# Optimization experiments

Measured on AMD Instinct MI355X. Metric: run time of the kernel, lower is better.

The kernel has to match this reference:

```python
import jax, jax.numpy as jnp
import numpy as np

N = 8192          # num atoms
APM = 32          # atoms per molecule
M = N // APM      # 256 molecules
FEAT = 100        # hidden_channels == num_filters
NG = 25           # num gaussians
K = 28            # knn neighbors
L = 4             # num interaction blocks
CUTOFF = 6.0
LOG2 = float(np.log(2.0))


def ssp(x):
    # pyg ShiftedSoftplus: softplus(x) - log(2)
    return jax.nn.softplus(x) - LOG2


def setup_inputs() -> dict:
    key = jax.random.key(0)
    ks = jax.random.split(key, 16)
    z = jax.random.randint(ks[0], (N,), 1, 100)
    pos = jax.random.normal(ks[1], (N, 3), jnp.float32) * 2.0
    ptr = jnp.arange(0, N + APM, APM)  # [M+1] molecule boundaries

    def w(k, shape, fan):
        return (jax.random.normal(k, shape, jnp.float32) / np.sqrt(fan)).astype(jnp.float32)

    def b(k, shape):
        return jax.random.normal(k, shape, jnp.float32) * 0.01

    kb = jax.random.split(ks[15], 8)
    H = FEAT // 2
    return {
        "z": z,
        "pos": pos,
        "ptr": ptr,
        "emb": jax.random.normal(ks[2], (100, FEAT), jnp.float32),
        "mlp_w1": w(ks[3], (L, NG, FEAT), NG),
        "mlp_b1": b(kb[0], (L, FEAT)),
        "mlp_w2": w(ks[4], (L, FEAT, FEAT), FEAT),
        "mlp_b2": b(kb[1], (L, FEAT)),
        "lin1_w": w(ks[5], (L, FEAT, FEAT), FEAT),
        "lin2_w": w(ks[6], (L, FEAT, FEAT), FEAT),
        "lin2_b": b(kb[2], (L, FEAT)),
        "lin_w": w(ks[7], (L, FEAT, FEAT), FEAT),
        "lin_b": b(kb[3], (L, FEAT)),
        "out_w1": w(ks[8], (FEAT, H), FEAT),
        "out_b1": b(kb[4], (H,)),
        "out_w2": w(ks[9], (H, 1), H),
        "out_b2": b(kb[5], (1,)),
    }


def reference(z, pos, ptr, emb, mlp_w1, mlp_b1, mlp_w2, mlp_b2,
              lin1_w, lin2_w, lin2_b, lin_w, lin_b,
              out_w1, out_b1, out_w2, out_b2):
    n = z.shape[0]
    m = ptr.shape[0] - 1

    # ptr -> per-atom batch ids (index_fill + cumsum; OOB index N dropped)
    flag = jnp.zeros((n,), jnp.int32).at[ptr].set(1, mode="drop")
    flag = flag.at[0].set(0)
    batch = jnp.cumsum(flag)

    # ---- KNN interaction graph (full NxN pairwise distances + masking + topk)
    diff = pos[:, None, :] - pos[None, :, :]           # [N,N,3]
    d2 = jnp.sum(diff * diff, axis=-1)                  # [N,N]
    ar = jnp.arange(n)
    mask = (ar[:, None] == ar[None, :]) \
         | (batch[:, None] != batch[None, :]) \
         | (d2 > CUTOFF * CUTOFF)
    dist = jnp.where(mask, CUTOFF, jnp.sqrt(jnp.where(mask, 1.0, d2)))
    neg, idx = jax.lax.top_k(-dist, K)                  # k nearest per row
    ew = -neg.reshape(-1)                               # edge distances [N*K]
    src = idx.reshape(-1)                               # source atoms j; target of edge (i,m) is i

    # ---- Gaussian smearing
    offset = jnp.linspace(0.0, CUTOFF, NG)
    coeff = -0.5 / (offset[1] - offset[0]) ** 2
    ea = jnp.exp(coeff * (ew[:, None] - offset[None, :]) ** 2)  # [E,NG]

    # cosine cutoff (zero weight for padded edges at dist==cutoff)
    ccut = 0.5 * (jnp.cos(ew * jnp.pi / CUTOFF) + 1.0)          # [E]

    h = emb[z]                                                   # [N,F]
    f = h.shape[1]
    for l in range(L):
        # filter network on edge attributes
        Wf = ssp(ea @ mlp_w1[l] + mlp_b1[l]) @ mlp_w2[l] + mlp_b2[l]
        Wf = Wf * ccut[:, None]                                  # [E,F]
        # CFConv: lin1 -> gather*filter -> sum over k neighbors -> lin2
        x1 = h @ lin1_w[l]                                       # [N,F]
        msg = x1[src] * Wf                                       # [E,F]
        agg = msg.reshape(n, K, f).sum(axis=1)                   # each node i has exactly K incoming edges
        v = ssp(agg @ lin2_w[l] + lin2_b[l]) @ lin_w[l] + lin_b[l]
        h = h + v

    # readout head
    h = ssp(h @ out_w1 + out_b1)
    per_atom = (h @ out_w2 + out_b2).reshape(-1)                 # [N]
    return jax.ops.segment_sum(per_atom, batch, num_segments=m) # per-molecule energy [M]
```

## Files before the change

### kernel.cpp

```cpp
#include <hip/hip_runtime.h>
#include <math.h>

#define APM   32
#define NMOL  256
#define FEAT  100
#define NPAD  112
#define LAYERS 4
#define NTHREADS 1024
#define NWAVES   16
#define G_TBL 4096
#define TROW  128
#define X1STR 132
#define KEDGE 28

typedef _Float16 f16x8 __attribute__((ext_vector_type(8)));
typedef _Float16 f16x2 __attribute__((ext_vector_type(2)));
typedef float    f32x4 __attribute__((ext_vector_type(4)));
typedef float    f32x2 __attribute__((ext_vector_type(2)));

#define L1F_OFF 0
#define L2F_OFF 14336
#define LVF_OFF 28672
#define LWTOT   43008
#define WTOTAL  (4*LWTOT)

#define PREP_BLOCKS 672
#define TBL_BLOCKS  256

__device__ __forceinline__ float sspf(float x){
  return __logf(1.0f + __expf(x)) - 0.69314718056f;
}

__global__ __launch_bounds__(256) void prep_all(
    const float* __restrict__ lin1_w, const float* __restrict__ lin2_w,
    const float* __restrict__ lin_w,
    const float* __restrict__ mlp_w1, const float* __restrict__ mlp_b1,
    const float* __restrict__ mlp_w2, const float* __restrict__ mlp_b2,
    _Float16* __restrict__ outw, _Float16* __restrict__ tbn)
{
  if (blockIdx.x < PREP_BLOCKS){
    int gid = blockIdx.x*256 + threadIdx.x;
    int l = gid / LWTOT;
    int r = gid - l*LWTOT;
    const float* W; int e;
    if (r < 14336)      { W = lin1_w + l*10000; e = r; }
    else if (r < 28672) { W = lin2_w + l*10000; e = r - 14336; }
    else                { W = lin_w  + l*10000; e = r - 28672; }
    int j = e & 7, L = (e >> 3) & 63, tile = e >> 9;
    int kc = tile / 7, nt = tile - kc*7;
    int k = kc*32 + ((L >> 4) << 3) + j;
    int f = nt*16 + (L & 15);
    float v = (k < 100 && f < FEAT) ? W[k*FEAT + f] : 0.0f;
    outw[gid] = (_Float16)v;
    return;
  }
  __shared__ float sW2[10000];
  __shared__ float sW1[2500];
  __shared__ float sB1[100], sB2[100];
  __shared__ float sT[4][100];
  int bid = blockIdx.x - PREP_BLOCKS;
  int l = bid >> 6;
  int s0 = (bid & 63) * 64;
  int tid = threadIdx.x, wv = tid >> 6, lane = tid & 63;
  for (int i = tid; i < 10000; i += 256) sW2[i] = mlp_w2[l*10000 + i];
  for (int i = tid; i < 2500;  i += 256) sW1[i] = mlp_w1[l*2500 + i];
  if (tid < 100) sB1[tid] = mlp_b1[l*100 + tid];
  if (tid >= 128 && tid < 228) sB2[tid-128] = mlp_b2[l*100 + tid-128];
  __syncthreads();
  #pragma unroll 1
  for (int si = 0; si < 16; si++){
    int s = s0 + wv*16 + si;
    float d = 6.0f * (float)s / (float)(G_TBL - 1);
    float ea[25];
    #pragma unroll
    for (int g = 0; g < 25; g++){
      float u = d - 0.25f*(float)g;
      ea[g] = __expf(-8.0f*u*u);
    }
    #pragma unroll
    for (int kk = 0; kk < 2; kk++){
      int k = lane + kk*64;
      if (k < 100){
        float acc = sB1[k];
        #pragma unroll
        for (int g = 0; g < 25; g++)
          acc += ea[g] * sW1[g*100 + k];
        sT[wv][k] = sspf(acc);
      }
    }
    float cc = 0.5f*(__cosf(d*0.52359877559f) + 1.0f);
    #pragma unroll
    for (int ff = 0; ff < 2; ff++){
      int f = lane + ff*64;
      float val = 0.0f;
      if (f < 100){
        float o0=0.0f, o1=0.0f, o2=0.0f, o3=0.0f;
        #pragma unroll
        for (int k = 0; k < 100; k += 4){
          o0 += sT[wv][k  ] * sW2[(k  )*100 + f];
          o1 += sT[wv][k+1] * sW2[(k+1)*100 + f];
          o2 += sT[wv][k+2] * sW2[(k+2)*100 + f];
          o3 += sT[wv][k+3] * sW2[(k+3)*100 + f];
        }
        val = (sB2[f] + ((o0+o1)+(o2+o3))) * cc;
      }
      tbn[((size_t)l*G_TBL + s)*TROW + f] = (_Float16)val;
    }
  }
}

__global__ __launch_bounds__(1024)
__attribute__((amdgpu_waves_per_eu(4, 4)))
void schnet_mega(
    const int* __restrict__ z, const float* __restrict__ pos,
    const float* __restrict__ emb, const _Float16* __restrict__ wf,
    const _Float16* __restrict__ tbn,
    const float* __restrict__ lin2_b, const float* __restrict__ lin_b,
    const float* __restrict__ out_w1, const float* __restrict__ out_b1,
    const float* __restrict__ out_w2, const float* __restrict__ out_b2,
    float* __restrict__ out)
{
  __shared__ __align__(16) _Float16 sAf[APM*136];
  __shared__ __align__(16) _Float16 sBf[APM*136];
  __shared__ __align__(16) float    sX1[APM*X1STR];
  __shared__ __align__(16) float    sH [APM*NPAD];
  __shared__ float sD  [APM*33];
  __shared__ int   sOffC[APM*KEDGE];
  __shared__ int   sJx  [APM*KEDGE];
  __shared__ float sPos[96];
  __shared__ float sPart[NWAVES];

  int tid = threadIdx.x, lane = tid & 63, wv = tid >> 6;
  int q = lane >> 4, n = lane & 15;
  int mol = blockIdx.x, mb = mol*APM;

  if (tid < 96) sPos[tid] = pos[mb*3 + tid];
  if (tid < 512){
    int r0 = tid >> 4, c0 = 112 + (tid & 15);
    sBf[r0*136 + c0] = (_Float16)0.0f;
  }
  for (int i = tid; i < APM*20; i += NTHREADS){
    int r = i/20, c = 112 + (i - r*20);
    sX1[r*X1STR + c] = 0.0f;
  }
  for (int i = tid; i < APM*136; i += NTHREADS){
    int r = i/136, c = i - r*136;
    float v = (c < FEAT) ? emb[z[mb+r]*FEAT + c] : 0.0f;
    sAf[i] = (_Float16)v;
    if (c < NPAD) sH[r*NPAD + c] = v;
  }
  __syncthreads();
  for (int p = tid; p < APM*APM; p += NTHREADS){
    int i = p >> 5, j = p & 31;
    float dx = sPos[i*3+0]-sPos[j*3+0];
    float dy = sPos[i*3+1]-sPos[j*3+1];
    float dz = sPos[i*3+2]-sPos[j*3+2];
    float d2 = dx*dx + dy*dy + dz*dz;
    sD[i*33+j] = (d2 > 36.0f) ? 6.0f : sqrtf(d2);
  }
  __syncthreads();
  if (tid < APM){
    float dd[32];
    #pragma unroll
    for (int j = 0; j < 32; j++) dd[j] = sD[tid*33+j];
    dd[tid] = 1e30f;
    unsigned dropped = 0u;
    for (int rr = 0; rr < 4; rr++){
      float mx = -1.0f; int mj = 0;
      #pragma unroll
      for (int j = 0; j < 32; j++){
        bool ok = !((dropped>>j)&1u) && (dd[j] > mx);
        mx = ok ? dd[j] : mx;  mj = ok ? j : mj;
      }
      dropped |= 1u << mj;
    }
    int e = 0;
    for (int j = 0; j < 32; j++){
      if ((dropped>>j)&1u) continue;
      float un = dd[j] * (float)((G_TBL-1)/6.0);
      int s = (int)(un + 0.5f);
      s = (s > G_TBL-1) ? (G_TBL-1) : s;
      sOffC[tid*KEDGE + e] = s*TROW;
      sJx  [tid*KEDGE + e] = j;
      e++;
    }
  }
  __syncthreads();

  for (int l = 0; l < LAYERS; l++){
    const _Float16* w1b = wf + l*LWTOT + L1F_OFF;
    const _Float16* w2b = wf + l*LWTOT + L2F_OFF;
    const _Float16* wvb = wf + l*LWTOT + LVF_OFF;
    const _Float16* tb = tbn + (size_t)l*G_TBL*TROW;
    for (int tau = wv; tau < 14; tau += NWAVES){
      int mt = tau/7, nt = tau - mt*7;
      f32x4 acc = {0.0f,0.0f,0.0f,0.0f};
      #pragma unroll
      for (int kc = 0; kc < 4; kc++){
        f16x8 av = *(const f16x8*)&sAf[(mt*16+n)*136 + kc*32 + q*8];
        f16x8 bv = *(const f16x8*)&w1b[((kc*7+nt)*64 + lane)*8];
        acc = __builtin_amdgcn_mfma_f32_16x16x32_f16(av, bv, acc, 0, 0, 0);
      }
      #pragma unroll
      for (int r = 0; r < 4; r++)
        sX1[(mt*16+q*4+r)*X1STR + nt*16+n] = acc[r];
    }
    __syncthreads();
    {
      int half = lane >> 5, L2i = (lane & 31)*2;
      int a = wv*2 + half, ar = a*KEDGE;
      float ag0=0.0f, ag1=0.0f, ag2=0.0f, ag3=0.0f;
      f16x2 PA[4][2]; int jA[4];
      f16x2 PB[4][2]; int jB[4];

#define GLD(E0, P, JV)                                                 \
      { _Pragma("unroll")                                              \
        for (int u = 0; u < 4; u++){                                   \
          int e = ar + (E0) + u;                                       \
          const _Float16* rp = tb + (sOffC[e] + L2i);                  \
          JV[u] = sJx[e];                                              \
          P[u][0] = *(const f16x2*)rp;                                 \
          P[u][1] = *(const f16x2*)(rp + 64);                          \
        } }
#define GCMP(P, JV)                                                    \
      { _Pragma("unroll")                                              \
        for (int u = 0; u < 4; u++){                                   \
          const float* xp = &sX1[JV[u]*X1STR + L2i];                   \
          f32x2 x0 = *(const f32x2*)xp;                                \
          f32x2 x1v = *(const f32x2*)(xp + 64);                        \
          ag0 += (float)P[u][0].x * x0.x;                              \
          ag1 += (float)P[u][0].y * x0.y;                              \
          ag2 += (float)P[u][1].x * x1v.x;                             \
          ag3 += (float)P[u][1].y * x1v.y;                             \
        } }

      GLD(0, PA, jA)
      #pragma unroll
      for (int b = 0; b < 7; b += 2){
        if (b+1 < 7) GLD((b+1)*4, PB, jB)
        GCMP(PA, jA)
        if (b+2 < 7) GLD((b+2)*4, PA, jA)
        if (b+1 < 7) GCMP(PB, jB)
      }
#undef GLD
#undef GCMP
      *(f16x2*)&sAf[a*136 + L2i]      = (f16x2){(_Float16)ag0,(_Float16)ag1};
      *(f16x2*)&sAf[a*136 + 64 + L2i] = (f16x2){(_Float16)ag2,(_Float16)ag3};
    }
    __syncthreads();
    for (int tau = wv; tau < 14; tau += NWAVES){
      int mt = tau/7, nt = tau - mt*7;
      f32x4 acc = {0.0f,0.0f,0.0f,0.0f};
      #pragma unroll
      for (int kc = 0; kc < 4; kc++){
        f16x8 av = *(const f16x8*)&sAf[(mt*16+n)*136 + kc*32 + q*8];
        f16x8 bv = *(const f16x8*)&w2b[((kc*7+nt)*64 + lane)*8];
        acc = __builtin_amdgcn_mfma_f32_16x16x32_f16(av, bv, acc, 0, 0, 0);
      }
      int f = nt*16 + n;
      float bb = (f < FEAT) ? lin2_b[l*FEAT + f] : 0.0f;
      #pragma unroll
      for (int r = 0; r < 4; r++)
        sBf[(mt*16+q*4+r)*136 + f] = (_Float16)sspf(acc[r] + bb);
    }
    __syncthreads();
    for (int tau = wv; tau < 14; tau += NWAVES){
      int mt = tau/7, nt = tau - mt*7;
      f32x4 acc = {0.0f,0.0f,0.0f,0.0f};
      #pragma unroll
      for (int kc = 0; kc < 4; kc++){
        f16x8 av = *(const f16x8*)&sBf[(mt*16+n)*136 + kc*32 + q*8];
        f16x8 bv = *(const f16x8*)&wvb[((kc*7+nt)*64 + lane)*8];
        acc = __builtin_amdgcn_mfma_f32_16x16x32_f16(av, bv, acc, 0, 0, 0);
      }
      int f = nt*16 + n;
      if (f < FEAT){
        float bb = lin_b[l*FEAT + f];
        #pragma unroll
        for (int r = 0; r < 4; r++){
          int row = mt*16 + q*4 + r;
          float hn = sH[row*NPAD + f] + acc[r] + bb;
          sH[row*NPAD + f] = hn;
          sAf[row*136 + f] = (_Float16)hn;
        }
      }
    }
    __syncthreads();
  }

  float ob2 = out_b2[0];
  float partial = 0.0f;
  for (int t = 0; t < 2; t++){
    int a = wv*2 + t;
    float u = 0.0f;
    if (lane < 50){
      u = out_b1[lane];
      #pragma unroll 4
      for (int c = 0; c < FEAT; c++)
        u += sH[a*NPAD + c] * out_w1[c*50 + lane];
      u = sspf(u) * out_w2[lane];
    }
    #pragma unroll
    for (int s = 1; s < 64; s <<= 1) u += __shfl_xor(u, s);
    partial += u + ob2;
  }
  if (lane == 0) sPart[wv] = partial;
  __syncthreads();
  if (tid == 0){
    float s = 0.0f;
    #pragma unroll
    for (int i = 0; i < NWAVES; i++) s += sPart[i];
    out[mol] = s;
  }
}

extern "C" void kernel_launch(void* const* d_in, const int* in_sizes, int n_in,
                              void* d_out, int out_size, void* d_ws, size_t ws_size,
                              hipStream_t stream)
{
  const int*   z      = (const int*)  d_in[0];
  const float* pos    = (const float*)d_in[1];
  const float* emb    = (const float*)d_in[3];
  const float* mlp_w1 = (const float*)d_in[4];
  const float* mlp_b1 = (const float*)d_in[5];
  const float* mlp_w2 = (const float*)d_in[6];
  const float* mlp_b2 = (const float*)d_in[7];
  const float* lin1_w = (const float*)d_in[8];
  const float* lin2_w = (const float*)d_in[9];
  const float* lin2_b = (const float*)d_in[10];
  const float* lin_w  = (const float*)d_in[11];
  const float* lin_b  = (const float*)d_in[12];
  const float* out_w1 = (const float*)d_in[13];
  const float* out_b1 = (const float*)d_in[14];
  const float* out_w2 = (const float*)d_in[15];
  const float* out_b2 = (const float*)d_in[16];

  _Float16* wfrag = (_Float16*)d_ws;
  _Float16* tbn   = (_Float16*)((char*)d_ws + WTOTAL*2);

  prep_all<<<PREP_BLOCKS + TBL_BLOCKS, 256, 0, stream>>>(
      lin1_w, lin2_w, lin_w, mlp_w1, mlp_b1, mlp_w2, mlp_b2, wfrag, tbn);
  schnet_mega<<<NMOL, NTHREADS, 0, stream>>>(z, pos, emb, wfrag, tbn,
      lin2_b, lin_b, out_w1, out_b1, out_w2, out_b2, (float*)d_out);
}
```

Baseline: 172.7 us.

## Prefetch next GEMM weights into registers and deepen gather pipeline

Each of the 14 MFMA waves now keeps its B-operand weight fragments in registers and issues the global loads for the next GEMM stage (lin2, then lin, then next layer's lin1) right after the current MFMAs. This hides global weight-load latency behind the barrier and the gather phase. The edge gather goes from two to three staged buffers so more table loads are in flight. The prep table kernel is also spread over four times as many blocks with fewer rows each. The cost is higher register pressure, which may reduce occupancy or cause spills.

```diff
diff --git a/kernel.cpp b/kernel.cpp
--- a/kernel.cpp
+++ b/kernel.cpp
@@ -25,7 +25,7 @@
 #define WTOTAL  (4*LWTOT)
 
 #define PREP_BLOCKS 672
-#define TBL_BLOCKS  256
+#define TBL_BLOCKS  1024
 
 __device__ __forceinline__ float sspf(float x){
   return __logf(1.0f + __expf(x)) - 0.69314718056f;
@@ -59,8 +59,8 @@
   __shared__ float sB1[100], sB2[100];
   __shared__ float sT[4][100];
   int bid = blockIdx.x - PREP_BLOCKS;
-  int l = bid >> 6;
-  int s0 = (bid & 63) * 64;
+  int l = bid >> 8;
+  int s0 = (bid & 255) * 16;
   int tid = threadIdx.x, wv = tid >> 6, lane = tid & 63;
   for (int i = tid; i < 10000; i += 256) sW2[i] = mlp_w2[l*10000 + i];
   for (int i = tid; i < 2500;  i += 256) sW1[i] = mlp_w1[l*2500 + i];
@@ -68,8 +68,8 @@
   if (tid >= 128 && tid < 228) sB2[tid-128] = mlp_b2[l*100 + tid-128];
   __syncthreads();
   #pragma unroll 1
-  for (int si = 0; si < 16; si++){
-    int s = s0 + wv*16 + si;
+  for (int si = 0; si < 4; si++){
+    int s = s0 + wv*4 + si;
     float d = 6.0f * (float)s / (float)(G_TBL - 1);
     float ea[25];
     #pragma unroll
@@ -134,6 +134,13 @@
   int q = lane >> 4, n = lane & 15;
   int mol = blockIdx.x, mb = mol*APM;
 
+  bool gw = (wv < 14);
+  int mt = (wv < 14) ? wv/7 : 0, nt = (wv < 14) ? wv - (wv/7)*7 : 0;
+  int boff0 = ((0*7+nt)*64 + lane)*8;
+  int boff1 = ((1*7+nt)*64 + lane)*8;
+  int boff2 = ((2*7+nt)*64 + lane)*8;
+  int boff3 = ((3*7+nt)*64 + lane)*8;
+
   if (tid < 96) sPos[tid] = pos[mb*3 + tid];
   if (tid < 512){
     int r0 = tid >> 4, c0 = 112 + (tid & 15);
@@ -148,6 +155,13 @@
     float v = (c < FEAT) ? emb[z[mb+r]*FEAT + c] : 0.0f;
     sAf[i] = (_Float16)v;
     if (c < NPAD) sH[r*NPAD + c] = v;
+  }
+  f16x8 nb0, nb1, nb2, nb3;
+  if (gw){
+    nb0 = *(const f16x8*)&wf[L1F_OFF + boff0];
+    nb1 = *(const f16x8*)&wf[L1F_OFF + boff1];
+    nb2 = *(const f16x8*)&wf[L1F_OFF + boff2];
+    nb3 = *(const f16x8*)&wf[L1F_OFF + boff3];
   }
   __syncthreads();
   for (int p = tid; p < APM*APM; p += NTHREADS){
@@ -188,19 +202,27 @@
   __syncthreads();
 
   for (int l = 0; l < LAYERS; l++){
-    const _Float16* w1b = wf + l*LWTOT + L1F_OFF;
     const _Float16* w2b = wf + l*LWTOT + L2F_OFF;
     const _Float16* wvb = wf + l*LWTOT + LVF_OFF;
+    const _Float16* w1n = wf + ((l+1)&3)*LWTOT + L1F_OFF;
     const _Float16* tb = tbn + (size_t)l*G_TBL*TROW;
-    for (int tau = wv; tau < 14; tau += NWAVES){
-      int mt = tau/7, nt = tau - mt*7;
+    if (gw){
       f32x4 acc = {0.0f,0.0f,0.0f,0.0f};
-      #pragma unroll
-      for (int kc = 0; kc < 4; kc++){
-        f16x8 av = *(const f16x8*)&sAf[(mt*16+n)*136 + kc*32 + q*8];
-        f16x8 bv = *(const f16x8*)&w1b[((kc*7+nt)*64 + lane)*8];
-        acc = __builtin_amdgcn_mfma_f32_16x16x32_f16(av, bv, acc, 0, 0, 0);
-      }
+      {
+        f16x8 av;
+        av = *(const f16x8*)&sAf[(mt*16+n)*136 + 0*32 + q*8];
+        acc = __builtin_amdgcn_mfma_f32_16x16x32_f16(av, nb0, acc, 0, 0, 0);
+        av = *(const f16x8*)&sAf[(mt*16+n)*136 + 1*32 + q*8];
+        acc = __builtin_amdgcn_mfma_f32_16x16x32_f16(av, nb1, acc, 0, 0, 0);
+        av = *(const f16x8*)&sAf[(mt*16+n)*136 + 2*32 + q*8];
+        acc = __builtin_amdgcn_mfma_f32_16x16x32_f16(av, nb2, acc, 0, 0, 0);
+        av = *(const f16x8*)&sAf[(mt*16+n)*136 + 3*32 + q*8];
+        acc = __builtin_amdgcn_mfma_f32_16x16x32_f16(av, nb3, acc, 0, 0, 0);
+      }
+      nb0 = *(const f16x8*)&w2b[boff0];
+      nb1 = *(const f16x8*)&w2b[boff1];
+      nb2 = *(const f16x8*)&w2b[boff2];
+      nb3 = *(const f16x8*)&w2b[boff3];
       #pragma unroll
       for (int r = 0; r < 4; r++)
         sX1[(mt*16+q*4+r)*X1STR + nt*16+n] = acc[r];
@@ -212,6 +234,7 @@
       float ag0=0.0f, ag1=0.0f, ag2=0.0f, ag3=0.0f;
       f16x2 PA[4][2]; int jA[4];
       f16x2 PB[4][2]; int jB[4];
+      f16x2 PC[4][2]; int jC[4];
 
 #define GLD(E0, P, JV)                                                 \
       { _Pragma("unroll")                                              \
@@ -234,29 +257,39 @@
           ag3 += (float)P[u][1].y * x1v.y;                             \
         } }
 
-      GLD(0, PA, jA)
-      #pragma unroll
-      for (int b = 0; b < 7; b += 2){
-        if (b+1 < 7) GLD((b+1)*4, PB, jB)
-        GCMP(PA, jA)
-        if (b+2 < 7) GLD((b+2)*4, PA, jA)
-        if (b+1 < 7) GCMP(PB, jB)
-      }
+      GLD(0,  PA, jA)
+      GLD(4,  PB, jB)
+      GLD(8,  PC, jC)
+      GCMP(PA, jA)  GLD(12, PA, jA)
+      GCMP(PB, jB)  GLD(16, PB, jB)
+      GCMP(PC, jC)  GLD(20, PC, jC)
+      GCMP(PA, jA)  GLD(24, PA, jA)
+      GCMP(PB, jB)
+      GCMP(PC, jC)
+      GCMP(PA, jA)
 #undef GLD
 #undef GCMP
       *(f16x2*)&sAf[a*136 + L2i]      = (f16x2){(_Float16)ag0,(_Float16)ag1};
       *(f16x2*)&sAf[a*136 + 64 + L2i] = (f16x2){(_Float16)ag2,(_Float16)ag3};
     }
     __syncthreads();
-    for (int tau = wv; tau < 14; tau += NWAVES){
-      int mt = tau/7, nt = tau - mt*7;
+    if (gw){
       f32x4 acc = {0.0f,0.0f,0.0f,0.0f};
-      #pragma unroll
-      for (int kc = 0; kc < 4; kc++){
-        f16x8 av = *(const f16x8*)&sAf[(mt*16+n)*136 + kc*32 + q*8];
-        f16x8 bv = *(const f16x8*)&w2b[((kc*7+nt)*64 + lane)*8];
-        acc = __builtin_amdgcn_mfma_f32_16x16x32_f16(av, bv, acc, 0, 0, 0);
-      }
+      {
+        f16x8 av;
+        av = *(const f16x8*)&sAf[(mt*16+n)*136 + 0*32 + q*8];
+        acc = __builtin_amdgcn_mfma_f32_16x16x32_f16(av, nb0, acc, 0, 0, 0);
+        av = *(const f16x8*)&sAf[(mt*16+n)*136 + 1*32 + q*8];
+        acc = __builtin_amdgcn_mfma_f32_16x16x32_f16(av, nb1, acc, 0, 0, 0);
+        av = *(const f16x8*)&sAf[(mt*16+n)*136 + 2*32 + q*8];
+        acc = __builtin_amdgcn_mfma_f32_16x16x32_f16(av, nb2, acc, 0, 0, 0);
+        av = *(const f16x8*)&sAf[(mt*16+n)*136 + 3*32 + q*8];
+        acc = __builtin_amdgcn_mfma_f32_16x16x32_f16(av, nb3, acc, 0, 0, 0);
+      }
+      nb0 = *(const f16x8*)&wvb[boff0];
+      nb1 = *(const f16x8*)&wvb[boff1];
+      nb2 = *(const f16x8*)&wvb[boff2];
+      nb3 = *(const f16x8*)&wvb[boff3];
       int f = nt*16 + n;
       float bb = (f < FEAT) ? lin2_b[l*FEAT + f] : 0.0f;
       #pragma unroll
@@ -264,15 +297,23 @@
         sBf[(mt*16+q*4+r)*136 + f] = (_Float16)sspf(acc[r] + bb);
     }
     __syncthreads();
-    for (int tau = wv; tau < 14; tau += NWAVES){
-      int mt = tau/7, nt = tau - mt*7;
+    if (gw){
       f32x4 acc = {0.0f,0.0f,0.0f,0.0f};
-      #pragma unroll
-      for (int kc = 0; kc < 4; kc++){
-        f16x8 av = *(const f16x8*)&sBf[(mt*16+n)*136 + kc*32 + q*8];
-        f16x8 bv = *(const f16x8*)&wvb[((kc*7+nt)*64 + lane)*8];
-        acc = __builtin_amdgcn_mfma_f32_16x16x32_f16(av, bv, acc, 0, 0, 0);
-      }
+      {
+        f16x8 av;
+        av = *(const f16x8*)&sBf[(mt*16+n)*136 + 0*32 + q*8];
+        acc = __builtin_amdgcn_mfma_f32_16x16x32_f16(av, nb0, acc, 0, 0, 0);
+        av = *(const f16x8*)&sBf[(mt*16+n)*136 + 1*32 + q*8];
+        acc = __builtin_amdgcn_mfma_f32_16x16x32_f16(av, nb1, acc, 0, 0, 0);
+        av = *(const f16x8*)&sBf[(mt*16+n)*136 + 2*32 + q*8];
+        acc = __builtin_amdgcn_mfma_f32_16x16x32_f16(av, nb2, acc, 0, 0, 0);
+        av = *(const f16x8*)&sBf[(mt*16+n)*136 + 3*32 + q*8];
+        acc = __builtin_amdgcn_mfma_f32_16x16x32_f16(av, nb3, acc, 0, 0, 0);
+      }
+      nb0 = *(const f16x8*)&w1n[boff0];
+      nb1 = *(const f16x8*)&w1n[boff1];
+      nb2 = *(const f16x8*)&w1n[boff2];
+      nb3 = *(const f16x8*)&w1n[boff3];
       int f = nt*16 + n;
       if (f < FEAT){
         float bb = lin_b[l*FEAT + f];
```

New measurement: 236.7 us. 37.1% more time.
